# Performance work log

Measured on AMD Instinct MI355X. Metric: run time of the kernel, lower is better.

## Reference

```python
import jax, jax.numpy as jnp
import numpy as np

OUT_H = 7
OUT_W = 7
SPATIAL_SCALE = 0.25
SAMPLING_RATIO = 2  # exact sampling branch (sampling_ratio > 0)
ALIGNED = True


def setup_inputs() -> dict:
    key = jax.random.key(0)
    k1, k2, k3, k4 = jax.random.split(key, 4)
    feat = jax.random.normal(k1, (4, 256, 100, 100), dtype=jnp.float32)
    # rois[K,5]: (batch_idx, x1, y1, x2, y2) in image coords (image ~400px since scale=0.25)
    K = 512
    bidx = jax.random.randint(k2, (K,), 0, 4).astype(jnp.float32)
    xy1 = jax.random.uniform(k3, (K, 2), minval=0.0, maxval=300.0, dtype=jnp.float32)
    wh = jax.random.uniform(k4, (K, 2), minval=20.0, maxval=99.0, dtype=jnp.float32)
    xy2 = xy1 + wh
    rois = jnp.concatenate([bidx[:, None], xy1[:, 0:1], xy1[:, 1:2], xy2[:, 0:1], xy2[:, 1:2]], axis=1)
    return {"input": feat, "rois": rois}


def _roi_align(feat, rois):
    N, C, H, W = feat.shape
    b = rois[:, 0].astype(jnp.int32)  # [K]
    offset = 0.5 if ALIGNED else 0.0
    sw = rois[:, 1] * SPATIAL_SCALE - offset
    sh = rois[:, 2] * SPATIAL_SCALE - offset
    ew = rois[:, 3] * SPATIAL_SCALE - offset
    eh = rois[:, 4] * SPATIAL_SCALE - offset
    rw = ew - sw
    rh = eh - sh
    if not ALIGNED:
        rw = jnp.maximum(rw, 1.0)
        rh = jnp.maximum(rh, 1.0)
    bin_h = rh / OUT_H  # [K]
    bin_w = rw / OUT_W

    ph = jnp.arange(OUT_H, dtype=feat.dtype)
    pw = jnp.arange(OUT_W, dtype=feat.dtype)
    samp = jnp.arange(SAMPLING_RATIO, dtype=feat.dtype) + 0.5  # (i + 0.5)

    # y: [K, OUT_H, SR], x: [K, OUT_W, SR]
    y = sh[:, None, None] + ph[None, :, None] * bin_h[:, None, None] + samp[None, None, :] * (bin_h / SAMPLING_RATIO)[:, None, None]
    x = sw[:, None, None] + pw[None, :, None] * bin_w[:, None, None] + samp[None, None, :] * (bin_w / SAMPLING_RATIO)[:, None, None]

    # bilinear interpolation indices/weights (matches _bilinear_interpolate)
    y = jnp.maximum(y, 0.0)
    x = jnp.maximum(x, 0.0)
    yl = y.astype(jnp.int32)
    xl = x.astype(jnp.int32)
    yh = jnp.where(yl >= H - 1, H - 1, yl + 1)
    yl = jnp.where(yl >= H - 1, H - 1, yl)
    xh = jnp.where(xl >= W - 1, W - 1, xl + 1)
    xl = jnp.where(xl >= W - 1, W - 1, xl)
    ly = y - yl.astype(feat.dtype)
    lx = x - xl.astype(feat.dtype)
    hy = 1.0 - ly
    hx = 1.0 - lx

    def gather(yi, xi):
        # yi: [K,PH,IY], xi: [K,PW,IX] -> [K,PH,IY,PW,IX,C]
        return feat[b[:, None, None, None, None], :,
                    yi[:, :, :, None, None],
                    xi[:, None, None, :, :]]

    v1 = gather(yl, xl)
    v2 = gather(yl, xh)
    v3 = gather(yh, xl)
    v4 = gather(yh, xh)

    out = (jnp.einsum('kpi,kqj,kpiqjc->kcpq', hy, hx, v1)
           + jnp.einsum('kpi,kqj,kpiqjc->kcpq', hy, lx, v2)
           + jnp.einsum('kpi,kqj,kpiqjc->kcpq', ly, hx, v3)
           + jnp.einsum('kpi,kqj,kpiqjc->kcpq', ly, lx, v4))
    count = float(max(SAMPLING_RATIO * SAMPLING_RATIO, 1))
    return out / count  # [K, C, OUT_H, OUT_W]


def reference(input, rois):
    return _roi_align(input, rois)
```

## Files before the change

kernel.cpp:

```cpp
#include <hip/hip_runtime.h>


#define FEAT_C 256
#define FEAT_H 100
#define FEAT_W 100
#define HW     10000
#define NROI   512
#define NBINS  49
#define CPI    4
#define ITEMS  8
#define PROWS  25
#define PSTR   28
#define CBYTES (PROWS * PSTR * 4)
#define BUFDW  (CPI * PROWS * PSTR)
#define BUFBYTES (BUFDW * 4)

__device__ __forceinline__ void samp_geo(float s, float bsz, int idx, int sr_i,
                                         int& lo, float& fr) {
    float v = s + bsz * ((float)idx + ((float)sr_i + 0.5f) * 0.5f);
    v = fmaxf(v, 0.0f);
    int l = (int)v;
    if (l > FEAT_H - 1) l = FEAT_H - 1;
    fr = v - (float)l;
    lo = l;
}

__global__ __launch_bounds__(256, 7) void roialign_fwd(
    const float* __restrict__ feat,
    const float* __restrict__ rois,
    float* __restrict__ out)
{
    __shared__ __align__(16) float s_patch[2 * BUFDW];
    __shared__ __align__(16) int2  s_yt[14];
    __shared__ __align__(16) int2  s_xt[14];

    const int bid  = blockIdx.x;
    const int k    = bid >> 3;
    const int cgrp = bid & 7;
    const int tid  = threadIdx.x;

    const float* r = rois + k * 5;
    const int   b  = (int)r[0];
    const float sw = r[1] * 0.25f - 0.5f, sh = r[2] * 0.25f - 0.5f;
    const float ew = r[3] * 0.25f - 0.5f, eh = r[4] * 0.25f - 0.5f;
    const float bh = (eh - sh) * (1.0f / 7.0f);
    const float bw = (ew - sw) * (1.0f / 7.0f);

    int y0, yM, x0, xM; float fd;
    samp_geo(sh, bh, 0, 0, y0, fd);  samp_geo(sh, bh, 6, 1, yM, fd);
    samp_geo(sw, bw, 0, 0, x0, fd);  samp_geo(sw, bw, 6, 1, xM, fd);
    const int ax0  = x0 & ~3;
    const int rows = yM - y0 + 2;

    if (tid < 14) {
        int lo; float fr;
        samp_geo(sh, bh, tid >> 1, tid & 1, lo, fr);
        s_yt[tid] = make_int2((lo - y0) * (PSTR * 4), __float_as_int(fr));
    } else if (tid >= 32 && tid < 46) {
        int t = tid - 32; int lo; float fr;
        samp_geo(sw, bw, t >> 1, t & 1, lo, fr);
        if (lo >= FEAT_W - 1) fr = 0.0f;
        s_xt[t] = make_int2((lo - ax0) * 4, __float_as_int(fr));
    }

    const int  spy = (tid * 9363) >> 16;
    const int  sq  = tid - spy * 7;
    int sy = y0 + spy; if (sy > FEAT_H - 1) sy = FEAT_H - 1;
    int sc = ax0 + sq * 4; if (sc > FEAT_W - 4) sc = FEAT_W - 4;
    const int  goff   = sy * FEAT_W + sc;
    const bool stager = tid < rows * 7;
    const int  wid    = __builtin_amdgcn_readfirstlane(tid >> 6);
    const float* fblk = feat + (size_t)(b * FEAT_C + cgrp * 32) * HW;

    auto dma = [&](int item, int selb) {
        if (stager) {
            const float* g0 = fblk + (size_t)item * (CPI * HW) + goff;
            char* l0 = (char*)s_patch + selb * BUFBYTES + wid * 1024;
            #pragma unroll
            for (int c = 0; c < CPI; c++)
                __builtin_amdgcn_global_load_lds(
                    (const __attribute__((address_space(1))) void*)(g0 + c * HW),
                    (__attribute__((address_space(3))) void*)(l0 + c * CBYTES),
                    16, 0, 0);
        }
    };

    dma(0, 0);
    __syncthreads();

    const int cch  = (tid * 335) >> 14;
    const int cbin = tid - cch * 49;
    const int cph  = (cbin * 37) >> 8;
    const int cpw  = cbin - cph * 7;
    const int4 yg = *(const int4*)&s_yt[2 * cph];
    const int4 xg = *(const int4*)&s_xt[2 * cpw];
    const float lyA = __int_as_float(yg.y), hyA = 1.0f - lyA;
    const float lyB = __int_as_float(yg.w), hyB = 1.0f - lyB;
    const float lx0 = __int_as_float(xg.y), hx0 = 1.0f - lx0;
    const float lx1 = __int_as_float(xg.w), hx1 = 1.0f - lx1;
    const int   choff = cch * CBYTES;
    float* const oblk = out + (size_t)(k * FEAT_C + cgrp * 32) * NBINS;

    int sel = 0;
    #pragma unroll
    for (int i = 0; i < ITEMS; i++) {
        if (i < ITEMS - 1) dma(i + 1, sel ^ 1);

        if (tid < CPI * NBINS) {
            const char* cb  = (const char*)s_patch + sel * BUFBYTES + choff;
            const char* rA  = cb + yg.x;
            const char* rB  = cb + yg.z;
            const float* a00 = (const float*)(rA + xg.x);
            const float* a01 = (const float*)(rA + xg.z);
            const float* a10 = (const float*)(rA + PSTR * 4 + xg.x);
            const float* a11 = (const float*)(rA + PSTR * 4 + xg.z);
            const float* b00 = (const float*)(rB + xg.x);
            const float* b01 = (const float*)(rB + xg.z);
            const float* b10 = (const float*)(rB + PSTR * 4 + xg.x);
            const float* b11 = (const float*)(rB + PSTR * 4 + xg.z);
            float loA = hx0 * a00[0] + lx0 * a00[1] + hx1 * a01[0] + lx1 * a01[1];
            float hiA = hx0 * a10[0] + lx0 * a10[1] + hx1 * a11[0] + lx1 * a11[1];
            float loB = hx0 * b00[0] + lx0 * b00[1] + hx1 * b01[0] + lx1 * b01[1];
            float hiB = hx0 * b10[0] + lx0 * b10[1] + hx1 * b11[0] + lx1 * b11[1];
            float acc = hyA * loA + lyA * hiA + hyB * loB + lyB * hiB;
            oblk[i * (CPI * NBINS) + tid] = acc * 0.25f;
        }

        if (i < ITEMS - 1) __syncthreads();
        sel ^= 1;
    }
}

extern "C" void kernel_launch(void* const* d_in, const int* in_sizes, int n_in,
                              void* d_out, int out_size, void* d_ws, size_t ws_size,
                              hipStream_t stream) {
    const float* feat = (const float*)d_in[0];
    const float* rois = (const float*)d_in[1];
    float*       outp = (float*)d_out;
    roialign_fwd<<<dim3(NROI * 8), dim3(256), 0, stream>>>(feat, rois, outp);
}
```

Before: 109.4 us.

## Stage whole feature channel in LDS and process all image ROIs per block

The old kernel had one block per ROI and channel group, staging a small patch for each. The new version adds a setup kernel that buckets ROIs by image and writes precomputed bilinear offsets and weights into workspace. The main kernel then loads one full 100x100 channel plane per (image, channel) block into LDS and evaluates every bin of every ROI in that image. Each feature element is read from global memory at most once, instead of once per overlapping ROI. The cost is a second launch, about 40KB of LDS per block that limits occupancy, scattered output stores, and uneven work across images.

```diff
diff --git a/kernel.cpp b/kernel.cpp
--- a/kernel.cpp
+++ b/kernel.cpp
@@ -7,13 +7,11 @@
 #define HW     10000
 #define NROI   512
 #define NBINS  49
-#define CPI    4
-#define ITEMS  8
-#define PROWS  25
-#define PSTR   28
-#define CBYTES (PROWS * PSTR * 4)
-#define BUFDW  (CPI * PROWS * PSTR)
-#define BUFBYTES (BUFDW * 4)
+#define IMG_N  4
+
+#define REC_BYTES  32
+#define IMG_STRIDE (NROI * NBINS * REC_BYTES)
+#define CNT_OFF    (IMG_N * IMG_STRIDE)
 
 __device__ __forceinline__ void samp_geo(float s, float bsz, int idx, int sr_i,
                                          int& lo, float& fr) {
@@ -25,109 +23,128 @@
     lo = l;
 }
 
-__global__ __launch_bounds__(256, 7) void roialign_fwd(
-    const float* __restrict__ feat,
-    const float* __restrict__ rois,
+__global__ __launch_bounds__(64) void roialign_setup(
+    const float* __restrict__ rois, char* __restrict__ ws)
+{
+    const int k    = blockIdx.x;
+    const int lane = threadIdx.x;
+    const float* r = rois + k * 5;
+    const int bk   = (int)r[0];
+
+    int slot = 0, total = 0;
+    for (int i = 0; i < NROI; i += 64) {
+        int bi = (int)rois[(i + lane) * 5];
+        unsigned long long m = __ballot(bi == bk);
+        total += __popcll(m);
+        int rel = k - i;
+        unsigned long long lt = rel <= 0 ? 0ull
+                              : (rel >= 64 ? ~0ull : ((1ull << rel) - 1ull));
+        slot += __popcll(m & lt);
+    }
+    if (lane == 0) ((int*)(ws + CNT_OFF))[bk] = total;
+
+    if (lane < NBINS) {
+        const float sw = r[1] * 0.25f - 0.5f, sh = r[2] * 0.25f - 0.5f;
+        const float ew = r[3] * 0.25f - 0.5f, eh = r[4] * 0.25f - 0.5f;
+        const float bh = (eh - sh) * (1.0f / 7.0f);
+        const float bw = (ew - sw) * (1.0f / 7.0f);
+        const int ph = (lane * 37) >> 8;
+        const int pw = lane - ph * 7;
+        int ylA, ylB, xl0, xl1; float lyA, lyB, lx0, lx1;
+        samp_geo(sh, bh, ph, 0, ylA, lyA);
+        samp_geo(sh, bh, ph, 1, ylB, lyB);
+        samp_geo(sw, bw, pw, 0, xl0, lx0);
+        samp_geo(sw, bw, pw, 1, xl1, lx1);
+        if (xl0 >= FEAT_W - 1) lx0 = 0.0f;
+        if (xl1 >= FEAT_W - 1) lx1 = 0.0f;
+        int yhA = min(ylA + 1, FEAT_H - 1), yhB = min(ylB + 1, FEAT_H - 1);
+        uint4 a, b2;
+        a.x  = (unsigned)(ylA * 400) | ((unsigned)(yhA * 400) << 16);
+        a.y  = (unsigned)(ylB * 400) | ((unsigned)(yhB * 400) << 16);
+        a.z  = (unsigned)(xl0 * 4)   | ((unsigned)(xl1 * 4)   << 16);
+        a.w  = __float_as_uint(lyA);
+        b2.x = __float_as_uint(lyB);
+        b2.y = __float_as_uint(lx0);
+        b2.z = __float_as_uint(lx1);
+        b2.w = (unsigned)(k * (FEAT_C * NBINS) + lane);
+        char* dst = ws + bk * IMG_STRIDE + (slot * NBINS + lane) * REC_BYTES;
+        *(uint4*)dst        = a;
+        *(uint4*)(dst + 16) = b2;
+    }
+}
+
+__global__ __launch_bounds__(256) void roialign_main(
+    const float* __restrict__ feat, const char* __restrict__ ws,
     float* __restrict__ out)
 {
-    __shared__ __align__(16) float s_patch[2 * BUFDW];
-    __shared__ __align__(16) int2  s_yt[14];
-    __shared__ __align__(16) int2  s_xt[14];
+    __shared__ __align__(16) float s_img[HW + 4];
 
     const int bid  = blockIdx.x;
-    const int k    = bid >> 3;
-    const int cgrp = bid & 7;
+    const int img  = bid & 3;
+    const int c    = bid >> 2;
     const int tid  = threadIdx.x;
+    const int lane = tid & 63;
+    const int w    = __builtin_amdgcn_readfirstlane(tid >> 6);
 
-    const float* r = rois + k * 5;
-    const int   b  = (int)r[0];
-    const float sw = r[1] * 0.25f - 0.5f, sh = r[2] * 0.25f - 0.5f;
-    const float ew = r[3] * 0.25f - 0.5f, eh = r[4] * 0.25f - 0.5f;
-    const float bh = (eh - sh) * (1.0f / 7.0f);
-    const float bw = (ew - sw) * (1.0f / 7.0f);
+    const char* src = (const char*)(feat + (size_t)(img * FEAT_C + c) * HW);
+    for (int j = w; j < 40; j += 4) {
+        int off = j * 1024 + lane * 16;
+        if (off < HW * 4)
+            __builtin_amdgcn_global_load_lds(
+                (const __attribute__((address_space(1))) void*)(src + off),
+                (__attribute__((address_space(3))) void*)((char*)s_img + off),
+                16, 0, 0);
+    }
+    if (tid < 4) s_img[HW + tid] = 0.0f;
 
-    int y0, yM, x0, xM; float fd;
-    samp_geo(sh, bh, 0, 0, y0, fd);  samp_geo(sh, bh, 6, 1, yM, fd);
-    samp_geo(sw, bw, 0, 0, x0, fd);  samp_geo(sw, bw, 6, 1, xM, fd);
-    const int ax0  = x0 & ~3;
-    const int rows = yM - y0 + 2;
+    const int   nrec = ((const int*)(ws + CNT_OFF))[img] * NBINS;
+    const char* rb   = ws + img * IMG_STRIDE;
+    float* const oc  = out + (size_t)c * NBINS;
 
-    if (tid < 14) {
-        int lo; float fr;
-        samp_geo(sh, bh, tid >> 1, tid & 1, lo, fr);
-        s_yt[tid] = make_int2((lo - y0) * (PSTR * 4), __float_as_int(fr));
-    } else if (tid >= 32 && tid < 46) {
-        int t = tid - 32; int lo; float fr;
-        samp_geo(sw, bw, t >> 1, t & 1, lo, fr);
-        if (lo >= FEAT_W - 1) fr = 0.0f;
-        s_xt[t] = make_int2((lo - ax0) * 4, __float_as_int(fr));
+    int   idx = tid;
+    uint4 ra, rbk;
+    if (idx < nrec) {
+        const char* p = rb + idx * REC_BYTES;
+        ra  = *(const uint4*)p;
+        rbk = *(const uint4*)(p + 16);
     }
-
-    const int  spy = (tid * 9363) >> 16;
-    const int  sq  = tid - spy * 7;
-    int sy = y0 + spy; if (sy > FEAT_H - 1) sy = FEAT_H - 1;
-    int sc = ax0 + sq * 4; if (sc > FEAT_W - 4) sc = FEAT_W - 4;
-    const int  goff   = sy * FEAT_W + sc;
-    const bool stager = tid < rows * 7;
-    const int  wid    = __builtin_amdgcn_readfirstlane(tid >> 6);
-    const float* fblk = feat + (size_t)(b * FEAT_C + cgrp * 32) * HW;
-
-    auto dma = [&](int item, int selb) {
-        if (stager) {
-            const float* g0 = fblk + (size_t)item * (CPI * HW) + goff;
-            char* l0 = (char*)s_patch + selb * BUFBYTES + wid * 1024;
-            #pragma unroll
-            for (int c = 0; c < CPI; c++)
-                __builtin_amdgcn_global_load_lds(
-                    (const __attribute__((address_space(1))) void*)(g0 + c * HW),
-                    (__attribute__((address_space(3))) void*)(l0 + c * CBYTES),
-                    16, 0, 0);
-        }
-    };
-
-    dma(0, 0);
     __syncthreads();
 
-    const int cch  = (tid * 335) >> 14;
-    const int cbin = tid - cch * 49;
-    const int cph  = (cbin * 37) >> 8;
-    const int cpw  = cbin - cph * 7;
-    const int4 yg = *(const int4*)&s_yt[2 * cph];
-    const int4 xg = *(const int4*)&s_xt[2 * cpw];
-    const float lyA = __int_as_float(yg.y), hyA = 1.0f - lyA;
-    const float lyB = __int_as_float(yg.w), hyB = 1.0f - lyB;
-    const float lx0 = __int_as_float(xg.y), hx0 = 1.0f - lx0;
-    const float lx1 = __int_as_float(xg.w), hx1 = 1.0f - lx1;
-    const int   choff = cch * CBYTES;
-    float* const oblk = out + (size_t)(k * FEAT_C + cgrp * 32) * NBINS;
-
-    int sel = 0;
-    #pragma unroll
-    for (int i = 0; i < ITEMS; i++) {
-        if (i < ITEMS - 1) dma(i + 1, sel ^ 1);
-
-        if (tid < CPI * NBINS) {
-            const char* cb  = (const char*)s_patch + sel * BUFBYTES + choff;
-            const char* rA  = cb + yg.x;
-            const char* rB  = cb + yg.z;
-            const float* a00 = (const float*)(rA + xg.x);
-            const float* a01 = (const float*)(rA + xg.z);
-            const float* a10 = (const float*)(rA + PSTR * 4 + xg.x);
-            const float* a11 = (const float*)(rA + PSTR * 4 + xg.z);
-            const float* b00 = (const float*)(rB + xg.x);
-            const float* b01 = (const float*)(rB + xg.z);
-            const float* b10 = (const float*)(rB + PSTR * 4 + xg.x);
-            const float* b11 = (const float*)(rB + PSTR * 4 + xg.z);
-            float loA = hx0 * a00[0] + lx0 * a00[1] + hx1 * a01[0] + lx1 * a01[1];
-            float hiA = hx0 * a10[0] + lx0 * a10[1] + hx1 * a11[0] + lx1 * a11[1];
-            float loB = hx0 * b00[0] + lx0 * b00[1] + hx1 * b01[0] + lx1 * b01[1];
-            float hiB = hx0 * b10[0] + lx0 * b10[1] + hx1 * b11[0] + lx1 * b11[1];
-            float acc = hyA * loA + lyA * hiA + hyB * loB + lyB * hiB;
-            oblk[i * (CPI * NBINS) + tid] = acc * 0.25f;
+    while (idx < nrec) {
+        const uint4 a = ra, b2 = rbk;
+        const int nidx = idx + 256;
+        if (nidx < nrec) {
+            const char* p = rb + nidx * REC_BYTES;
+            ra  = *(const uint4*)p;
+            rbk = *(const uint4*)(p + 16);
         }
 
-        if (i < ITEMS - 1) __syncthreads();
-        sel ^= 1;
+        const char* base = (const char*)s_img;
+        const int oAl = a.x & 0xffff, oAh = a.x >> 16;
+        const int oBl = a.y & 0xffff, oBh = a.y >> 16;
+        const int x0  = a.z & 0xffff, x1  = a.z >> 16;
+        const float lyA = __uint_as_float(a.w),  hyA = 1.0f - lyA;
+        const float lyB = __uint_as_float(b2.x), hyB = 1.0f - lyB;
+        const float lx0 = __uint_as_float(b2.y), hx0 = 1.0f - lx0;
+        const float lx1 = __uint_as_float(b2.z), hx1 = 1.0f - lx1;
+
+        const float* pAl0 = (const float*)(base + oAl + x0);
+        const float* pAl1 = (const float*)(base + oAl + x1);
+        const float* pAh0 = (const float*)(base + oAh + x0);
+        const float* pAh1 = (const float*)(base + oAh + x1);
+        const float* pBl0 = (const float*)(base + oBl + x0);
+        const float* pBl1 = (const float*)(base + oBl + x1);
+        const float* pBh0 = (const float*)(base + oBh + x0);
+        const float* pBh1 = (const float*)(base + oBh + x1);
+
+        float sAl = hx0 * pAl0[0] + lx0 * pAl0[1] + hx1 * pAl1[0] + lx1 * pAl1[1];
+        float sAh = hx0 * pAh0[0] + lx0 * pAh0[1] + hx1 * pAh1[0] + lx1 * pAh1[1];
+        float sBl = hx0 * pBl0[0] + lx0 * pBl0[1] + hx1 * pBl1[0] + lx1 * pBl1[1];
+        float sBh = hx0 * pBh0[0] + lx0 * pBh0[1] + hx1 * pBh1[0] + lx1 * pBh1[1];
+        float acc = hyA * sAl + lyA * sAh + hyB * sBl + lyB * sBh;
+
+        oc[b2.w] = acc * 0.25f;
+        idx = nidx;
     }
 }
 
@@ -137,5 +154,7 @@
     const float* feat = (const float*)d_in[0];
     const float* rois = (const float*)d_in[1];
     float*       outp = (float*)d_out;
-    roialign_fwd<<<dim3(NROI * 8), dim3(256), 0, stream>>>(feat, rois, outp);
+    roialign_setup<<<dim3(NROI), dim3(64), 0, stream>>>(rois, (char*)d_ws);
+    roialign_main<<<dim3(IMG_N * FEAT_C), dim3(256), 0, stream>>>(
+        feat, (const char*)d_ws, outp);
 }
```

After: 102.6 us. -6.2%, faster.
